# Kernel optimization log

Measured on AMD Instinct MI355X. Metric: run time of the kernel, lower is better.

Reference implementation:

```python
import jax, jax.numpy as jnp
import numpy as np

MAX_ITER = 10
EPSILON = 1e-4
B, N1, N2 = 64, 1024, 1024


def setup_inputs() -> dict:
    key = jax.random.key(0)
    k_s, k_r, k_c = jax.random.split(key, 3)
    s = jax.random.uniform(k_s, (B, N1, N2), dtype=jnp.float32)
    nrows = jax.random.randint(k_r, (B,), 512, N1 + 1, dtype=jnp.int32)
    ncols = jax.random.randint(k_c, (B,), 512, N2 + 1, dtype=jnp.int32)
    return {"s": s, "n1": N1, "n2": N2, "nrows": nrows, "ncols": ncols}


def reference(s, n1, n2, nrows, ncols):
    # s: [B, N1, N2] affinity; nrows/ncols: [B] valid sizes; n1/n2: static ints.
    b, r, c = s.shape
    row_mask = jnp.arange(r)[None, :] < nrows[:, None]          # [B, N1]
    col_mask = jnp.arange(c)[None, :] < ncols[:, None]          # [B, N2]
    valid = row_mask[:, :, None] & col_mask[:, None, :]         # [B, N1, N2]

    s = s + EPSILON
    # off-block zeroing (no-op when n1==N1, n2==N2, matching torch fill_(0))
    s = s.at[:, :n1, n2:].set(0.0)
    s = s.at[:, n1:, :n2].set(0.0)

    for i in range(MAX_ITER):
        if i % 2 == 1:
            # row sums over valid columns (s @ col_ones_block), broadcast over cols
            ssum = jnp.sum(jnp.where(col_mask[:, None, :], s, 0.0), axis=2, keepdims=True)
        else:
            # column sums over valid rows (row_ones_block @ s), broadcast over rows
            ssum = jnp.sum(jnp.where(row_mask[:, :, None], s, 0.0), axis=1, keepdims=True)
        denom = jnp.where(valid, jnp.broadcast_to(ssum, s.shape), 1.0)
        s = jnp.where(valid, s / denom, 0.0)  # tmp = 1/sum inside block, 0 outside
    return s
```

## Files before the change

### kernel.cpp

```cpp
#include <hip/hip_runtime.h>

#define EPS 1e-4f
#define BB 64
#define NN 1024

typedef _Float16 f16x8 __attribute__((ext_vector_type(8)));
typedef _Float16 f16x4 __attribute__((ext_vector_type(4)));

__global__ __launch_bounds__(256) void compress_colsum_k(
    const float* __restrict__ s, _Float16* __restrict__ A,
    const int* __restrict__ nrows, const int* __restrict__ ncols,
    float* __restrict__ partial)
{
    int chunk = blockIdx.x;
    int b = blockIdx.y;
    int nr = nrows[b], nc = ncols[b];
    int t = threadIdx.x;
    int j = t << 2;
    int i0 = chunk << 6;
    int i1 = min(i0 + 64, nr);
    const float* sb = s + ((size_t)b << 20) + j;
    _Float16* Ab = A + ((size_t)b << 20) + j;
    float a0 = 0.f, a1 = 0.f, a2 = 0.f, a3 = 0.f;
    if (j < nc) {
        for (int i = i0; i < i1; ++i) {
            float4 v = *(const float4*)(sb + ((size_t)i << 10));
            float m0 = (j + 0 < nc) ? v.x + EPS : 0.f;
            float m1 = (j + 1 < nc) ? v.y + EPS : 0.f;
            float m2 = (j + 2 < nc) ? v.z + EPS : 0.f;
            float m3 = (j + 3 < nc) ? v.w + EPS : 0.f;
            f16x4 h;
            h[0] = (_Float16)m0; h[1] = (_Float16)m1;
            h[2] = (_Float16)m2; h[3] = (_Float16)m3;
            a0 += (float)h[0]; a1 += (float)h[1];
            a2 += (float)h[2]; a3 += (float)h[3];
            *(f16x4*)(Ab + ((size_t)i << 10)) = h;
        }
    } else {
        f16x4 z = {};
        for (int i = i0; i < i1; ++i)
            *(f16x4*)(Ab + ((size_t)i << 10)) = z;
    }
    *(float4*)(partial + (((size_t)((chunk << 6) + b)) << 10) + j) =
        make_float4(a0, a1, a2, a3);
}

__global__ __launch_bounds__(256) void pair_k(
    const _Float16* __restrict__ A, const float* __restrict__ pin,
    const int* __restrict__ nrows, const int* __restrict__ ncols,
    float* __restrict__ pout)
{
    __shared__ float cs[NN];
    __shared__ float mg[4][NN];
    int chunk = blockIdx.x, b = blockIdx.y;
    int nr = nrows[b], nc = ncols[b];
    int t = threadIdx.x;
    {
        int j = t << 2;
        const float* pb = pin + ((size_t)b << 10) + j;
        float4 u = make_float4(0.f, 0.f, 0.f, 0.f);
#pragma unroll
        for (int k = 0; k < 16; ++k) {
            float4 p = *(const float4*)(pb + ((size_t)k << 16));
            u.x += p.x; u.y += p.y; u.z += p.z; u.w += p.w;
        }
        cs[j + 0] = (j + 0 < nc) ? 1.0f / u.x : 0.f;
        cs[j + 1] = (j + 1 < nc) ? 1.0f / u.y : 0.f;
        cs[j + 2] = (j + 2 < nc) ? 1.0f / u.z : 0.f;
        cs[j + 3] = (j + 3 < nc) ? 1.0f / u.w : 0.f;
    }
    __syncthreads();

    int w = t >> 6, lane = t & 63;
    int col0 = lane << 3;
    float4 c0a = *(const float4*)&cs[col0];
    float4 c0b = *(const float4*)&cs[col0 + 4];
    float4 c1a = *(const float4*)&cs[512 + col0];
    float4 c1b = *(const float4*)&cs[512 + col0 + 4];
    bool do1 = (512 + col0) < nc;

    float acc0[8] = {0.f, 0.f, 0.f, 0.f, 0.f, 0.f, 0.f, 0.f};
    float acc1[8] = {0.f, 0.f, 0.f, 0.f, 0.f, 0.f, 0.f, 0.f};
    const _Float16* Ab = A + ((size_t)b << 20);
    int i0 = chunk << 6;
    int iend = min(i0 + 64, nr);
    for (int i = i0 + w; i < iend; i += 4) {
        const _Float16* row = Ab + ((size_t)i << 10);
        f16x8 q0 = *(const f16x8*)(row + col0);
        f16x8 q1 = {};
        if (do1) q1 = *(const f16x8*)(row + 512 + col0);
        float f0[8], f1[8];
#pragma unroll
        for (int k = 0; k < 8; ++k) { f0[k] = (float)q0[k]; f1[k] = (float)q1[k]; }
        float sum = f0[0]*c0a.x + f0[1]*c0a.y + f0[2]*c0a.z + f0[3]*c0a.w
                  + f0[4]*c0b.x + f0[5]*c0b.y + f0[6]*c0b.z + f0[7]*c0b.w
                  + f1[0]*c1a.x + f1[1]*c1a.y + f1[2]*c1a.z + f1[3]*c1a.w
                  + f1[4]*c1b.x + f1[5]*c1b.y + f1[6]*c1b.z + f1[7]*c1b.w;
#pragma unroll
        for (int o = 32; o > 0; o >>= 1) sum += __shfl_xor(sum, o, 64);
        float ri = 1.0f / sum;
#pragma unroll
        for (int k = 0; k < 8; ++k) { acc0[k] += f0[k] * ri; acc1[k] += f1[k] * ri; }
    }
    *(float4*)&mg[w][col0]       = make_float4(acc0[0], acc0[1], acc0[2], acc0[3]);
    *(float4*)&mg[w][col0 + 4]   = make_float4(acc0[4], acc0[5], acc0[6], acc0[7]);
    *(float4*)&mg[w][512 + col0]     = make_float4(acc1[0], acc1[1], acc1[2], acc1[3]);
    *(float4*)&mg[w][512 + col0 + 4] = make_float4(acc1[4], acc1[5], acc1[6], acc1[7]);
    __syncthreads();
    int j = t << 2;
    float4 m = make_float4(0.f, 0.f, 0.f, 0.f);
#pragma unroll
    for (int ww = 0; ww < 4; ++ww) {
        float4 v = *(const float4*)&mg[ww][j];
        m.x += v.x; m.y += v.y; m.z += v.z; m.w += v.w;
    }
    *(float4*)(pout + (((size_t)((chunk << 6) + b)) << 10) + j) = m;
}

__global__ __launch_bounds__(256) void reduce_c_k(
    const float* __restrict__ partial, const int* __restrict__ ncols,
    float* __restrict__ c)
{
    int b = blockIdx.y;
    int j = (blockIdx.x << 8) + threadIdx.x;
    int nc = ncols[b];
    const float* pb = partial + ((size_t)b << 10) + j;
    float u = 0.f;
#pragma unroll
    for (int k = 0; k < 16; ++k) u += pb[(size_t)k << 16];
    c[(b << 10) + j] = (j < nc) ? 1.0f / u : 0.f;
}

__global__ __launch_bounds__(256) void finalize_k(
    const _Float16* __restrict__ A, const float* __restrict__ c,
    const int* __restrict__ nrows, float* __restrict__ out)
{
    __shared__ float red[4];
    int b = blockIdx.y, i = blockIdx.x;
    int nr = nrows[b];
    int t = threadIdx.x;
    int j = t << 2;
    size_t off = ((size_t)b << 20) + ((size_t)i << 10) + j;
    if (i >= nr) {
        *(float4*)(out + off) = make_float4(0.f, 0.f, 0.f, 0.f);
        return;
    }
    f16x4 h = *(const f16x4*)(A + off);
    float4 cv = *(const float4*)(c + (b << 10) + j);
    float4 p;
    p.x = (float)h[0] * cv.x;
    p.y = (float)h[1] * cv.y;
    p.z = (float)h[2] * cv.z;
    p.w = (float)h[3] * cv.w;
    float sum = (p.x + p.y) + (p.z + p.w);
#pragma unroll
    for (int o = 32; o > 0; o >>= 1) sum += __shfl_xor(sum, o, 64);
    int w = t >> 6, lane = t & 63;
    if (lane == 0) red[w] = sum;
    __syncthreads();
    float total = (red[0] + red[1]) + (red[2] + red[3]);
    float ri = 1.0f / total;
    *(float4*)(out + off) = make_float4(p.x * ri, p.y * ri, p.z * ri, p.w * ri);
}

extern "C" void kernel_launch(void* const* d_in, const int* in_sizes, int n_in,
                              void* d_out, int out_size, void* d_ws, size_t ws_size,
                              hipStream_t stream) {
    const float* s     = (const float*)d_in[0];
    const int*   nrows = (const int*)d_in[3];
    const int*   ncols = (const int*)d_in[4];
    float* out = (float*)d_out;

    _Float16* A  = (_Float16*)d_ws;
    float* pA    = (float*)((char*)d_ws + ((size_t)BB << 20) * sizeof(_Float16));
    float* pB    = pA + ((size_t)16 * BB * NN);
    float* c5    = pB + ((size_t)16 * BB * NN);

    compress_colsum_k<<<dim3(16, BB), 256, 0, stream>>>(s, A, nrows, ncols, pA);
    pair_k<<<dim3(16, BB), 256, 0, stream>>>(A, pA, nrows, ncols, pB);
    pair_k<<<dim3(16, BB), 256, 0, stream>>>(A, pB, nrows, ncols, pA);
    pair_k<<<dim3(16, BB), 256, 0, stream>>>(A, pA, nrows, ncols, pB);
    pair_k<<<dim3(16, BB), 256, 0, stream>>>(A, pB, nrows, ncols, pA);
    reduce_c_k<<<dim3(4, BB), 256, 0, stream>>>(pA, ncols, c5);
    finalize_k<<<dim3(NN, BB), 256, 0, stream>>>(A, c5, nrows, out);
}
```

Before: 565.3 us.

## Fuse final column reduction into finalize and process two rows per wave

Removes the separate reduce_c kernel by folding the partial column-sum reduction into a new finalize kernel that works on 64-row chunks per block, as pair_k does. The final pass now uses a 16x64 grid instead of 1024x64 blocks of one row each. Both pair_k and finalize process two rows per wave per iteration, interleaving the two shuffle reductions to expose more ILP and memory parallelism. The cost is more registers per thread, and each finalize block redundantly re-reduces the 16 partials.

```diff
diff --git a/kernel.cpp b/kernel.cpp
--- a/kernel.cpp
+++ b/kernel.cpp
@@ -84,26 +84,55 @@
     const _Float16* Ab = A + ((size_t)b << 20);
     int i0 = chunk << 6;
     int iend = min(i0 + 64, nr);
-    for (int i = i0 + w; i < iend; i += 4) {
-        const _Float16* row = Ab + ((size_t)i << 10);
-        f16x8 q0 = *(const f16x8*)(row + col0);
-        f16x8 q1 = {};
-        if (do1) q1 = *(const f16x8*)(row + 512 + col0);
-        float f0[8], f1[8];
-#pragma unroll
-        for (int k = 0; k < 8; ++k) { f0[k] = (float)q0[k]; f1[k] = (float)q1[k]; }
-        float sum = f0[0]*c0a.x + f0[1]*c0a.y + f0[2]*c0a.z + f0[3]*c0a.w
-                  + f0[4]*c0b.x + f0[5]*c0b.y + f0[6]*c0b.z + f0[7]*c0b.w
-                  + f1[0]*c1a.x + f1[1]*c1a.y + f1[2]*c1a.z + f1[3]*c1a.w
-                  + f1[4]*c1b.x + f1[5]*c1b.y + f1[6]*c1b.z + f1[7]*c1b.w;
-#pragma unroll
-        for (int o = 32; o > 0; o >>= 1) sum += __shfl_xor(sum, o, 64);
-        float ri = 1.0f / sum;
-#pragma unroll
-        for (int k = 0; k < 8; ++k) { acc0[k] += f0[k] * ri; acc1[k] += f1[k] * ri; }
-    }
-    *(float4*)&mg[w][col0]       = make_float4(acc0[0], acc0[1], acc0[2], acc0[3]);
-    *(float4*)&mg[w][col0 + 4]   = make_float4(acc0[4], acc0[5], acc0[6], acc0[7]);
+    for (int i = i0 + w; i < iend; i += 8) {
+        int ib = i + 4;
+        bool hasB = ib < iend;
+        const _Float16* rA = Ab + ((size_t)i << 10);
+        const _Float16* rB = Ab + ((size_t)(hasB ? ib : i) << 10);
+        f16x8 qa0 = *(const f16x8*)(rA + col0);
+        f16x8 qb0 = *(const f16x8*)(rB + col0);
+        f16x8 qa1 = {}; f16x8 qb1 = {};
+        if (do1) {
+            qa1 = *(const f16x8*)(rA + 512 + col0);
+            qb1 = *(const f16x8*)(rB + 512 + col0);
+        }
+        float fa0[8], fa1[8], fb0[8], fb1[8];
+#pragma unroll
+        for (int k = 0; k < 8; ++k) {
+            fa0[k] = (float)qa0[k]; fa1[k] = (float)qa1[k];
+            fb0[k] = (float)qb0[k]; fb1[k] = (float)qb1[k];
+        }
+        float sa, sb_;
+        {
+            float p0 = fa0[0]*c0a.x + fa0[1]*c0a.y + fa0[2]*c0a.z + fa0[3]*c0a.w;
+            float p1 = fa0[4]*c0b.x + fa0[5]*c0b.y + fa0[6]*c0b.z + fa0[7]*c0b.w;
+            float p2 = fa1[0]*c1a.x + fa1[1]*c1a.y + fa1[2]*c1a.z + fa1[3]*c1a.w;
+            float p3 = fa1[4]*c1b.x + fa1[5]*c1b.y + fa1[6]*c1b.z + fa1[7]*c1b.w;
+            sa = (p0 + p1) + (p2 + p3);
+        }
+        {
+            float p0 = fb0[0]*c0a.x + fb0[1]*c0a.y + fb0[2]*c0a.z + fb0[3]*c0a.w;
+            float p1 = fb0[4]*c0b.x + fb0[5]*c0b.y + fb0[6]*c0b.z + fb0[7]*c0b.w;
+            float p2 = fb1[0]*c1a.x + fb1[1]*c1a.y + fb1[2]*c1a.z + fb1[3]*c1a.w;
+            float p3 = fb1[4]*c1b.x + fb1[5]*c1b.y + fb1[6]*c1b.z + fb1[7]*c1b.w;
+            sb_ = (p0 + p1) + (p2 + p3);
+        }
+#pragma unroll
+        for (int o = 32; o > 0; o >>= 1) {
+            float ta = __shfl_xor(sa, o, 64);
+            float tb = __shfl_xor(sb_, o, 64);
+            sa += ta; sb_ += tb;
+        }
+        float ra = 1.0f / sa;
+        float rb = hasB ? (1.0f / sb_) : 0.f;
+#pragma unroll
+        for (int k = 0; k < 8; ++k) {
+            acc0[k] += fa0[k] * ra + fb0[k] * rb;
+            acc1[k] += fa1[k] * ra + fb1[k] * rb;
+        }
+    }
+    *(float4*)&mg[w][col0]           = make_float4(acc0[0], acc0[1], acc0[2], acc0[3]);
+    *(float4*)&mg[w][col0 + 4]       = make_float4(acc0[4], acc0[5], acc0[6], acc0[7]);
     *(float4*)&mg[w][512 + col0]     = make_float4(acc1[0], acc1[1], acc1[2], acc1[3]);
     *(float4*)&mg[w][512 + col0 + 4] = make_float4(acc1[4], acc1[5], acc1[6], acc1[7]);
     __syncthreads();
@@ -117,50 +146,116 @@
     *(float4*)(pout + (((size_t)((chunk << 6) + b)) << 10) + j) = m;
 }
 
-__global__ __launch_bounds__(256) void reduce_c_k(
-    const float* __restrict__ partial, const int* __restrict__ ncols,
-    float* __restrict__ c)
+__global__ __launch_bounds__(256) void finalize2_k(
+    const _Float16* __restrict__ A, const float* __restrict__ pin,
+    const int* __restrict__ nrows, const int* __restrict__ ncols,
+    float* __restrict__ out)
 {
-    int b = blockIdx.y;
-    int j = (blockIdx.x << 8) + threadIdx.x;
-    int nc = ncols[b];
-    const float* pb = partial + ((size_t)b << 10) + j;
-    float u = 0.f;
-#pragma unroll
-    for (int k = 0; k < 16; ++k) u += pb[(size_t)k << 16];
-    c[(b << 10) + j] = (j < nc) ? 1.0f / u : 0.f;
-}
-
-__global__ __launch_bounds__(256) void finalize_k(
-    const _Float16* __restrict__ A, const float* __restrict__ c,
-    const int* __restrict__ nrows, float* __restrict__ out)
-{
-    __shared__ float red[4];
-    int b = blockIdx.y, i = blockIdx.x;
-    int nr = nrows[b];
+    __shared__ float cs[NN];
+    int chunk = blockIdx.x, b = blockIdx.y;
+    int nr = nrows[b], nc = ncols[b];
     int t = threadIdx.x;
-    int j = t << 2;
-    size_t off = ((size_t)b << 20) + ((size_t)i << 10) + j;
-    if (i >= nr) {
-        *(float4*)(out + off) = make_float4(0.f, 0.f, 0.f, 0.f);
-        return;
-    }
-    f16x4 h = *(const f16x4*)(A + off);
-    float4 cv = *(const float4*)(c + (b << 10) + j);
-    float4 p;
-    p.x = (float)h[0] * cv.x;
-    p.y = (float)h[1] * cv.y;
-    p.z = (float)h[2] * cv.z;
-    p.w = (float)h[3] * cv.w;
-    float sum = (p.x + p.y) + (p.z + p.w);
-#pragma unroll
-    for (int o = 32; o > 0; o >>= 1) sum += __shfl_xor(sum, o, 64);
+    {
+        int j = t << 2;
+        const float* pb = pin + ((size_t)b << 10) + j;
+        float4 u = make_float4(0.f, 0.f, 0.f, 0.f);
+#pragma unroll
+        for (int k = 0; k < 16; ++k) {
+            float4 p = *(const float4*)(pb + ((size_t)k << 16));
+            u.x += p.x; u.y += p.y; u.z += p.z; u.w += p.w;
+        }
+        cs[j + 0] = (j + 0 < nc) ? 1.0f / u.x : 0.f;
+        cs[j + 1] = (j + 1 < nc) ? 1.0f / u.y : 0.f;
+        cs[j + 2] = (j + 2 < nc) ? 1.0f / u.z : 0.f;
+        cs[j + 3] = (j + 3 < nc) ? 1.0f / u.w : 0.f;
+    }
+    __syncthreads();
+
     int w = t >> 6, lane = t & 63;
-    if (lane == 0) red[w] = sum;
-    __syncthreads();
-    float total = (red[0] + red[1]) + (red[2] + red[3]);
-    float ri = 1.0f / total;
-    *(float4*)(out + off) = make_float4(p.x * ri, p.y * ri, p.z * ri, p.w * ri);
+    int col0 = lane << 3;
+    float4 c0a = *(const float4*)&cs[col0];
+    float4 c0b = *(const float4*)&cs[col0 + 4];
+    float4 c1a = *(const float4*)&cs[512 + col0];
+    float4 c1b = *(const float4*)&cs[512 + col0 + 4];
+    bool do1 = (512 + col0) < nc;
+
+    const _Float16* Ab = A + ((size_t)b << 20);
+    float* Ob = out + ((size_t)b << 20);
+    int i0 = chunk << 6;
+    int iend = min(i0 + 64, nr);
+    for (int i = i0 + w; i < iend; i += 8) {
+        int ib = i + 4;
+        bool hasB = ib < iend;
+        const _Float16* rA = Ab + ((size_t)i << 10);
+        const _Float16* rB = Ab + ((size_t)(hasB ? ib : i) << 10);
+        f16x8 qa0 = *(const f16x8*)(rA + col0);
+        f16x8 qb0 = *(const f16x8*)(rB + col0);
+        f16x8 qa1 = {}; f16x8 qb1 = {};
+        if (do1) {
+            qa1 = *(const f16x8*)(rA + 512 + col0);
+            qb1 = *(const f16x8*)(rB + 512 + col0);
+        }
+        float pa[16], pb2[16];
+        pa[0]  = (float)qa0[0]*c0a.x; pa[1]  = (float)qa0[1]*c0a.y;
+        pa[2]  = (float)qa0[2]*c0a.z; pa[3]  = (float)qa0[3]*c0a.w;
+        pa[4]  = (float)qa0[4]*c0b.x; pa[5]  = (float)qa0[5]*c0b.y;
+        pa[6]  = (float)qa0[6]*c0b.z; pa[7]  = (float)qa0[7]*c0b.w;
+        pa[8]  = (float)qa1[0]*c1a.x; pa[9]  = (float)qa1[1]*c1a.y;
+        pa[10] = (float)qa1[2]*c1a.z; pa[11] = (float)qa1[3]*c1a.w;
+        pa[12] = (float)qa1[4]*c1b.x; pa[13] = (float)qa1[5]*c1b.y;
+        pa[14] = (float)qa1[6]*c1b.z; pa[15] = (float)qa1[7]*c1b.w;
+        pb2[0]  = (float)qb0[0]*c0a.x; pb2[1]  = (float)qb0[1]*c0a.y;
+        pb2[2]  = (float)qb0[2]*c0a.z; pb2[3]  = (float)qb0[3]*c0a.w;
+        pb2[4]  = (float)qb0[4]*c0b.x; pb2[5]  = (float)qb0[5]*c0b.y;
+        pb2[6]  = (float)qb0[6]*c0b.z; pb2[7]  = (float)qb0[7]*c0b.w;
+        pb2[8]  = (float)qb1[0]*c1a.x; pb2[9]  = (float)qb1[1]*c1a.y;
+        pb2[10] = (float)qb1[2]*c1a.z; pb2[11] = (float)qb1[3]*c1a.w;
+        pb2[12] = (float)qb1[4]*c1b.x; pb2[13] = (float)qb1[5]*c1b.y;
+        pb2[14] = (float)qb1[6]*c1b.z; pb2[15] = (float)qb1[7]*c1b.w;
+        float sa, sb_;
+        {
+            float q0 = ((pa[0]+pa[1])+(pa[2]+pa[3])) + ((pa[4]+pa[5])+(pa[6]+pa[7]));
+            float q1 = ((pa[8]+pa[9])+(pa[10]+pa[11])) + ((pa[12]+pa[13])+(pa[14]+pa[15]));
+            sa = q0 + q1;
+        }
+        {
+            float q0 = ((pb2[0]+pb2[1])+(pb2[2]+pb2[3])) + ((pb2[4]+pb2[5])+(pb2[6]+pb2[7]));
+            float q1 = ((pb2[8]+pb2[9])+(pb2[10]+pb2[11])) + ((pb2[12]+pb2[13])+(pb2[14]+pb2[15]));
+            sb_ = q0 + q1;
+        }
+#pragma unroll
+        for (int o = 32; o > 0; o >>= 1) {
+            float ta = __shfl_xor(sa, o, 64);
+            float tb = __shfl_xor(sb_, o, 64);
+            sa += ta; sb_ += tb;
+        }
+        float ra = 1.0f / sa;
+        {
+            float* o = Ob + ((size_t)i << 10);
+            *(float4*)(o + col0)           = make_float4(pa[0]*ra,  pa[1]*ra,  pa[2]*ra,  pa[3]*ra);
+            *(float4*)(o + col0 + 4)       = make_float4(pa[4]*ra,  pa[5]*ra,  pa[6]*ra,  pa[7]*ra);
+            *(float4*)(o + 512 + col0)     = make_float4(pa[8]*ra,  pa[9]*ra,  pa[10]*ra, pa[11]*ra);
+            *(float4*)(o + 512 + col0 + 4) = make_float4(pa[12]*ra, pa[13]*ra, pa[14]*ra, pa[15]*ra);
+        }
+        if (hasB) {
+            float rb = 1.0f / sb_;
+            float* o = Ob + ((size_t)ib << 10);
+            *(float4*)(o + col0)           = make_float4(pb2[0]*rb,  pb2[1]*rb,  pb2[2]*rb,  pb2[3]*rb);
+            *(float4*)(o + col0 + 4)       = make_float4(pb2[4]*rb,  pb2[5]*rb,  pb2[6]*rb,  pb2[7]*rb);
+            *(float4*)(o + 512 + col0)     = make_float4(pb2[8]*rb,  pb2[9]*rb,  pb2[10]*rb, pb2[11]*rb);
+            *(float4*)(o + 512 + col0 + 4) = make_float4(pb2[12]*rb, pb2[13]*rb, pb2[14]*rb, pb2[15]*rb);
+        }
+    }
+    for (int i = i0 + w; i < i0 + 64; i += 4) {
+        if (i >= nr) {
+            float* o = Ob + ((size_t)i << 10);
+            float4 z = make_float4(0.f, 0.f, 0.f, 0.f);
+            *(float4*)(o + col0)           = z;
+            *(float4*)(o + col0 + 4)       = z;
+            *(float4*)(o + 512 + col0)     = z;
+            *(float4*)(o + 512 + col0 + 4) = z;
+        }
+    }
 }
 
 extern "C" void kernel_launch(void* const* d_in, const int* in_sizes, int n_in,
@@ -174,13 +269,11 @@
     _Float16* A  = (_Float16*)d_ws;
     float* pA    = (float*)((char*)d_ws + ((size_t)BB << 20) * sizeof(_Float16));
     float* pB    = pA + ((size_t)16 * BB * NN);
-    float* c5    = pB + ((size_t)16 * BB * NN);
 
     compress_colsum_k<<<dim3(16, BB), 256, 0, stream>>>(s, A, nrows, ncols, pA);
     pair_k<<<dim3(16, BB), 256, 0, stream>>>(A, pA, nrows, ncols, pB);
     pair_k<<<dim3(16, BB), 256, 0, stream>>>(A, pB, nrows, ncols, pA);
     pair_k<<<dim3(16, BB), 256, 0, stream>>>(A, pA, nrows, ncols, pB);
     pair_k<<<dim3(16, BB), 256, 0, stream>>>(A, pB, nrows, ncols, pA);
-    reduce_c_k<<<dim3(4, BB), 256, 0, stream>>>(pA, ncols, c5);
-    finalize_k<<<dim3(NN, BB), 256, 0, stream>>>(A, c5, nrows, out);
-}
+    finalize2_k<<<dim3(16, BB), 256, 0, stream>>>(A, pA, nrows, ncols, out);
+}
```

After: 567.9 us. No clear change (+0.4%).

## Fuse all Sinkhorn stages into one persistent kernel with grid barriers

Applied to the files above, without the earlier changes.

Replaces the seven separate kernel launches with a single persistent kernel of 256 blocks of 1024 threads (four blocks per batch). Stages are separated by atomic-counter grid barriers, and the final row normalisation is folded into the same kernel. The goal is to remove launch gaps and shrink the partial-sum buffers. In exchange it relies on all 256 blocks being co-resident, which risks deadlock otherwise, and it uses less parallelism per stage with spin-waits at each barrier.

```diff
diff --git a/kernel.cpp b/kernel.cpp
--- a/kernel.cpp
+++ b/kernel.cpp
@@ -7,160 +7,206 @@
 typedef _Float16 f16x8 __attribute__((ext_vector_type(8)));
 typedef _Float16 f16x4 __attribute__((ext_vector_type(4)));
 
-__global__ __launch_bounds__(256) void compress_colsum_k(
+__device__ __forceinline__ void grid_barrier(unsigned* bar, int slot,
+                                             unsigned nblk) {
+    __syncthreads();
+    if (threadIdx.x == 0) {
+        __threadfence();
+        __hip_atomic_fetch_add(&bar[slot], 1u, __ATOMIC_ACQ_REL,
+                               __HIP_MEMORY_SCOPE_AGENT);
+        while (__hip_atomic_load(&bar[slot], __ATOMIC_ACQUIRE,
+                                 __HIP_MEMORY_SCOPE_AGENT) < nblk) {
+            __builtin_amdgcn_s_sleep(8);
+        }
+        __threadfence();
+    }
+    __syncthreads();
+}
+
+__global__ __launch_bounds__(1024) void sinkhorn_fused(
     const float* __restrict__ s, _Float16* __restrict__ A,
     const int* __restrict__ nrows, const int* __restrict__ ncols,
-    float* __restrict__ partial)
+    float* __restrict__ p0, float* __restrict__ p1,
+    unsigned* __restrict__ bar, float* __restrict__ out)
 {
-    int chunk = blockIdx.x;
-    int b = blockIdx.y;
+    __shared__ float cs[NN];
+    __shared__ float mg[8][NN];
+
+    const unsigned NBLK = 256;
+    int g = blockIdx.x;
+    int q = g & 3, b = g >> 2;
     int nr = nrows[b], nc = ncols[b];
     int t = threadIdx.x;
-    int j = t << 2;
-    int i0 = chunk << 6;
-    int i1 = min(i0 + 64, nr);
-    const float* sb = s + ((size_t)b << 20) + j;
-    _Float16* Ab = A + ((size_t)b << 20) + j;
-    float a0 = 0.f, a1 = 0.f, a2 = 0.f, a3 = 0.f;
-    if (j < nc) {
-        for (int i = i0; i < i1; ++i) {
-            float4 v = *(const float4*)(sb + ((size_t)i << 10));
-            float m0 = (j + 0 < nc) ? v.x + EPS : 0.f;
-            float m1 = (j + 1 < nc) ? v.y + EPS : 0.f;
-            float m2 = (j + 2 < nc) ? v.z + EPS : 0.f;
-            float m3 = (j + 3 < nc) ? v.w + EPS : 0.f;
-            f16x4 h;
-            h[0] = (_Float16)m0; h[1] = (_Float16)m1;
-            h[2] = (_Float16)m2; h[3] = (_Float16)m3;
-            a0 += (float)h[0]; a1 += (float)h[1];
-            a2 += (float)h[2]; a3 += (float)h[3];
-            *(f16x4*)(Ab + ((size_t)i << 10)) = h;
-        }
-    } else {
-        f16x4 z = {};
-        for (int i = i0; i < i1; ++i)
-            *(f16x4*)(Ab + ((size_t)i << 10)) = z;
-    }
-    *(float4*)(partial + (((size_t)((chunk << 6) + b)) << 10) + j) =
-        make_float4(a0, a1, a2, a3);
-}
-
-__global__ __launch_bounds__(256) void pair_k(
-    const _Float16* __restrict__ A, const float* __restrict__ pin,
-    const int* __restrict__ nrows, const int* __restrict__ ncols,
-    float* __restrict__ pout)
-{
-    __shared__ float cs[NN];
-    __shared__ float mg[4][NN];
-    int chunk = blockIdx.x, b = blockIdx.y;
-    int nr = nrows[b], nc = ncols[b];
-    int t = threadIdx.x;
-    {
-        int j = t << 2;
-        const float* pb = pin + ((size_t)b << 10) + j;
-        float4 u = make_float4(0.f, 0.f, 0.f, 0.f);
-#pragma unroll
-        for (int k = 0; k < 16; ++k) {
-            float4 p = *(const float4*)(pb + ((size_t)k << 16));
-            u.x += p.x; u.y += p.y; u.z += p.z; u.w += p.w;
-        }
-        cs[j + 0] = (j + 0 < nc) ? 1.0f / u.x : 0.f;
-        cs[j + 1] = (j + 1 < nc) ? 1.0f / u.y : 0.f;
-        cs[j + 2] = (j + 2 < nc) ? 1.0f / u.z : 0.f;
-        cs[j + 3] = (j + 3 < nc) ? 1.0f / u.w : 0.f;
-    }
-    __syncthreads();
-
     int w = t >> 6, lane = t & 63;
     int col0 = lane << 3;
-    float4 c0a = *(const float4*)&cs[col0];
-    float4 c0b = *(const float4*)&cs[col0 + 4];
-    float4 c1a = *(const float4*)&cs[512 + col0];
-    float4 c1b = *(const float4*)&cs[512 + col0 + 4];
-    bool do1 = (512 + col0) < nc;
-
-    float acc0[8] = {0.f, 0.f, 0.f, 0.f, 0.f, 0.f, 0.f, 0.f};
-    float acc1[8] = {0.f, 0.f, 0.f, 0.f, 0.f, 0.f, 0.f, 0.f};
+    int tq = t >> 8, tj = t & 255;
+    int j4 = tj << 2;
     const _Float16* Ab = A + ((size_t)b << 20);
-    int i0 = chunk << 6;
-    int iend = min(i0 + 64, nr);
-    for (int i = i0 + w; i < iend; i += 4) {
-        const _Float16* row = Ab + ((size_t)i << 10);
-        f16x8 q0 = *(const f16x8*)(row + col0);
-        f16x8 q1 = {};
-        if (do1) q1 = *(const f16x8*)(row + 512 + col0);
-        float f0[8], f1[8];
-#pragma unroll
-        for (int k = 0; k < 8; ++k) { f0[k] = (float)q0[k]; f1[k] = (float)q1[k]; }
-        float sum = f0[0]*c0a.x + f0[1]*c0a.y + f0[2]*c0a.z + f0[3]*c0a.w
-                  + f0[4]*c0b.x + f0[5]*c0b.y + f0[6]*c0b.z + f0[7]*c0b.w
-                  + f1[0]*c1a.x + f1[1]*c1a.y + f1[2]*c1a.z + f1[3]*c1a.w
-                  + f1[4]*c1b.x + f1[5]*c1b.y + f1[6]*c1b.z + f1[7]*c1b.w;
-#pragma unroll
-        for (int o = 32; o > 0; o >>= 1) sum += __shfl_xor(sum, o, 64);
-        float ri = 1.0f / sum;
-#pragma unroll
-        for (int k = 0; k < 8; ++k) { acc0[k] += f0[k] * ri; acc1[k] += f1[k] * ri; }
-    }
-    *(float4*)&mg[w][col0]       = make_float4(acc0[0], acc0[1], acc0[2], acc0[3]);
-    *(float4*)&mg[w][col0 + 4]   = make_float4(acc0[4], acc0[5], acc0[6], acc0[7]);
-    *(float4*)&mg[w][512 + col0]     = make_float4(acc1[0], acc1[1], acc1[2], acc1[3]);
-    *(float4*)&mg[w][512 + col0 + 4] = make_float4(acc1[4], acc1[5], acc1[6], acc1[7]);
+    size_t poffQ = ((size_t)((q << 6) + b)) << 10;
+
+    {
+        int chunk = (q << 2) + tq;
+        int r0 = chunk << 6;
+        int r1 = min(r0 + 64, nr);
+        const float* sb = s + ((size_t)b << 20) + j4;
+        _Float16* Aw = A + ((size_t)b << 20) + j4;
+        float a0 = 0.f, a1 = 0.f, a2 = 0.f, a3 = 0.f;
+        if (j4 < nc) {
+            for (int i = r0; i < r1; ++i) {
+                float4 v = *(const float4*)(sb + ((size_t)i << 10));
+                float m0 = (j4 + 0 < nc) ? v.x + EPS : 0.f;
+                float m1 = (j4 + 1 < nc) ? v.y + EPS : 0.f;
+                float m2 = (j4 + 2 < nc) ? v.z + EPS : 0.f;
+                float m3 = (j4 + 3 < nc) ? v.w + EPS : 0.f;
+                f16x4 h;
+                h[0] = (_Float16)m0; h[1] = (_Float16)m1;
+                h[2] = (_Float16)m2; h[3] = (_Float16)m3;
+                a0 += (float)h[0]; a1 += (float)h[1];
+                a2 += (float)h[2]; a3 += (float)h[3];
+                *(f16x4*)(Aw + ((size_t)i << 10)) = h;
+            }
+        } else {
+            f16x4 z = {};
+            for (int i = r0; i < r1; ++i)
+                *(f16x4*)(Aw + ((size_t)i << 10)) = z;
+        }
+        *(float4*)&mg[tq][j4] = make_float4(a0, a1, a2, a3);
+        __syncthreads();
+        if (t < 256) {
+            int jj = t << 2;
+            float4 m = make_float4(0.f, 0.f, 0.f, 0.f);
+#pragma unroll
+            for (int k = 0; k < 4; ++k) {
+                float4 v = *(const float4*)&mg[k][jj];
+                m.x += v.x; m.y += v.y; m.z += v.z; m.w += v.w;
+            }
+            *(float4*)(p0 + poffQ + jj) = m;
+        }
+    }
+    grid_barrier(bar, 0, NBLK);
+
+    const float* pin = p0;
+    float* pout = p1;
+    for (int it = 0; it < 4; ++it) {
+        {
+            const float* pb = pin + ((size_t)b << 10) + t;
+            float u = 0.f;
+#pragma unroll
+            for (int k = 0; k < 4; ++k) u += pb[(size_t)k << 16];
+            cs[t] = (t < nc) ? 1.0f / u : 0.f;
+        }
+        __syncthreads();
+
+        float4 c0a = *(const float4*)&cs[col0];
+        float4 c0b = *(const float4*)&cs[col0 + 4];
+        float4 c1a = *(const float4*)&cs[512 + col0];
+        float4 c1b = *(const float4*)&cs[512 + col0 + 4];
+        bool do1 = (512 + col0) < nc;
+
+        float acc0[8] = {0.f, 0.f, 0.f, 0.f, 0.f, 0.f, 0.f, 0.f};
+        float acc1[8] = {0.f, 0.f, 0.f, 0.f, 0.f, 0.f, 0.f, 0.f};
+        int base = (q << 8) + (w << 4);
+        int iend = min(base + 16, nr);
+        for (int i = base; i < iend; ++i) {
+            const _Float16* row = Ab + ((size_t)i << 10);
+            f16x8 q0 = *(const f16x8*)(row + col0);
+            f16x8 q1 = {};
+            if (do1) q1 = *(const f16x8*)(row + 512 + col0);
+            float f0[8], f1[8];
+#pragma unroll
+            for (int k = 0; k < 8; ++k) { f0[k] = (float)q0[k]; f1[k] = (float)q1[k]; }
+            float p0s = f0[0]*c0a.x + f0[1]*c0a.y + f0[2]*c0a.z + f0[3]*c0a.w;
+            float p1s = f0[4]*c0b.x + f0[5]*c0b.y + f0[6]*c0b.z + f0[7]*c0b.w;
+            float p2s = f1[0]*c1a.x + f1[1]*c1a.y + f1[2]*c1a.z + f1[3]*c1a.w;
+            float p3s = f1[4]*c1b.x + f1[5]*c1b.y + f1[6]*c1b.z + f1[7]*c1b.w;
+            float sum = (p0s + p1s) + (p2s + p3s);
+#pragma unroll
+            for (int o = 32; o > 0; o >>= 1) sum += __shfl_xor(sum, o, 64);
+            float ri = 1.0f / sum;
+#pragma unroll
+            for (int k = 0; k < 8; ++k) { acc0[k] += f0[k] * ri; acc1[k] += f1[k] * ri; }
+        }
+        if (w >= 8) {
+            int ww = w - 8;
+            *(float4*)&mg[ww][col0]           = make_float4(acc0[0], acc0[1], acc0[2], acc0[3]);
+            *(float4*)&mg[ww][col0 + 4]       = make_float4(acc0[4], acc0[5], acc0[6], acc0[7]);
+            *(float4*)&mg[ww][512 + col0]     = make_float4(acc1[0], acc1[1], acc1[2], acc1[3]);
+            *(float4*)&mg[ww][512 + col0 + 4] = make_float4(acc1[4], acc1[5], acc1[6], acc1[7]);
+        }
+        __syncthreads();
+        if (w < 8) {
+            float4 v;
+            v = *(const float4*)&mg[w][col0];
+            *(float4*)&mg[w][col0]           = make_float4(v.x+acc0[0], v.y+acc0[1], v.z+acc0[2], v.w+acc0[3]);
+            v = *(const float4*)&mg[w][col0 + 4];
+            *(float4*)&mg[w][col0 + 4]       = make_float4(v.x+acc0[4], v.y+acc0[5], v.z+acc0[6], v.w+acc0[7]);
+            v = *(const float4*)&mg[w][512 + col0];
+            *(float4*)&mg[w][512 + col0]     = make_float4(v.x+acc1[0], v.y+acc1[1], v.z+acc1[2], v.w+acc1[3]);
+            v = *(const float4*)&mg[w][512 + col0 + 4];
+            *(float4*)&mg[w][512 + col0 + 4] = make_float4(v.x+acc1[4], v.y+acc1[5], v.z+acc1[6], v.w+acc1[7]);
+        }
+        __syncthreads();
+        {
+            float m = 0.f;
+#pragma unroll
+            for (int k = 0; k < 8; ++k) m += mg[k][t];
+            pout[poffQ + t] = m;
+        }
+        grid_barrier(bar, 1 + it, NBLK);
+        const float* tmp = pout; pout = (float*)pin; pin = tmp;
+    }
+
+    {
+        const float* pb = pin + ((size_t)b << 10) + t;
+        float u = 0.f;
+#pragma unroll
+        for (int k = 0; k < 4; ++k) u += pb[(size_t)k << 16];
+        cs[t] = (t < nc) ? 1.0f / u : 0.f;
+    }
     __syncthreads();
-    int j = t << 2;
-    float4 m = make_float4(0.f, 0.f, 0.f, 0.f);
-#pragma unroll
-    for (int ww = 0; ww < 4; ++ww) {
-        float4 v = *(const float4*)&mg[ww][j];
-        m.x += v.x; m.y += v.y; m.z += v.z; m.w += v.w;
-    }
-    *(float4*)(pout + (((size_t)((chunk << 6) + b)) << 10) + j) = m;
-}
-
-__global__ __launch_bounds__(256) void reduce_c_k(
-    const float* __restrict__ partial, const int* __restrict__ ncols,
-    float* __restrict__ c)
-{
-    int b = blockIdx.y;
-    int j = (blockIdx.x << 8) + threadIdx.x;
-    int nc = ncols[b];
-    const float* pb = partial + ((size_t)b << 10) + j;
-    float u = 0.f;
-#pragma unroll
-    for (int k = 0; k < 16; ++k) u += pb[(size_t)k << 16];
-    c[(b << 10) + j] = (j < nc) ? 1.0f / u : 0.f;
-}
-
-__global__ __launch_bounds__(256) void finalize_k(
-    const _Float16* __restrict__ A, const float* __restrict__ c,
-    const int* __restrict__ nrows, float* __restrict__ out)
-{
-    __shared__ float red[4];
-    int b = blockIdx.y, i = blockIdx.x;
-    int nr = nrows[b];
-    int t = threadIdx.x;
-    int j = t << 2;
-    size_t off = ((size_t)b << 20) + ((size_t)i << 10) + j;
-    if (i >= nr) {
-        *(float4*)(out + off) = make_float4(0.f, 0.f, 0.f, 0.f);
-        return;
-    }
-    f16x4 h = *(const f16x4*)(A + off);
-    float4 cv = *(const float4*)(c + (b << 10) + j);
-    float4 p;
-    p.x = (float)h[0] * cv.x;
-    p.y = (float)h[1] * cv.y;
-    p.z = (float)h[2] * cv.z;
-    p.w = (float)h[3] * cv.w;
-    float sum = (p.x + p.y) + (p.z + p.w);
-#pragma unroll
-    for (int o = 32; o > 0; o >>= 1) sum += __shfl_xor(sum, o, 64);
-    int w = t >> 6, lane = t & 63;
-    if (lane == 0) red[w] = sum;
-    __syncthreads();
-    float total = (red[0] + red[1]) + (red[2] + red[3]);
-    float ri = 1.0f / total;
-    *(float4*)(out + off) = make_float4(p.x * ri, p.y * ri, p.z * ri, p.w * ri);
+    {
+        float4 c0a = *(const float4*)&cs[col0];
+        float4 c0b = *(const float4*)&cs[col0 + 4];
+        float4 c1a = *(const float4*)&cs[512 + col0];
+        float4 c1b = *(const float4*)&cs[512 + col0 + 4];
+        bool do1 = (512 + col0) < nc;
+        float* Ob = out + ((size_t)b << 20);
+        int base = (q << 8) + (w << 4);
+        for (int i = base; i < base + 16; ++i) {
+            float* o = Ob + ((size_t)i << 10);
+            if (i < nr) {
+                const _Float16* row = Ab + ((size_t)i << 10);
+                f16x8 q0 = *(const f16x8*)(row + col0);
+                f16x8 q1 = {};
+                if (do1) q1 = *(const f16x8*)(row + 512 + col0);
+                float p[16];
+                p[0]  = (float)q0[0]*c0a.x; p[1]  = (float)q0[1]*c0a.y;
+                p[2]  = (float)q0[2]*c0a.z; p[3]  = (float)q0[3]*c0a.w;
+                p[4]  = (float)q0[4]*c0b.x; p[5]  = (float)q0[5]*c0b.y;
+                p[6]  = (float)q0[6]*c0b.z; p[7]  = (float)q0[7]*c0b.w;
+                p[8]  = (float)q1[0]*c1a.x; p[9]  = (float)q1[1]*c1a.y;
+                p[10] = (float)q1[2]*c1a.z; p[11] = (float)q1[3]*c1a.w;
+                p[12] = (float)q1[4]*c1b.x; p[13] = (float)q1[5]*c1b.y;
+                p[14] = (float)q1[6]*c1b.z; p[15] = (float)q1[7]*c1b.w;
+                float s0 = ((p[0]+p[1])+(p[2]+p[3])) + ((p[4]+p[5])+(p[6]+p[7]));
+                float s1 = ((p[8]+p[9])+(p[10]+p[11])) + ((p[12]+p[13])+(p[14]+p[15]));
+                float sum = s0 + s1;
+#pragma unroll
+                for (int o2 = 32; o2 > 0; o2 >>= 1) sum += __shfl_xor(sum, o2, 64);
+                float ri = 1.0f / sum;
+                *(float4*)(o + col0)           = make_float4(p[0]*ri,  p[1]*ri,  p[2]*ri,  p[3]*ri);
+                *(float4*)(o + col0 + 4)       = make_float4(p[4]*ri,  p[5]*ri,  p[6]*ri,  p[7]*ri);
+                *(float4*)(o + 512 + col0)     = make_float4(p[8]*ri,  p[9]*ri,  p[10]*ri, p[11]*ri);
+                *(float4*)(o + 512 + col0 + 4) = make_float4(p[12]*ri, p[13]*ri, p[14]*ri, p[15]*ri);
+            } else {
+                float4 z = make_float4(0.f, 0.f, 0.f, 0.f);
+                *(float4*)(o + col0)           = z;
+                *(float4*)(o + col0 + 4)       = z;
+                *(float4*)(o + 512 + col0)     = z;
+                *(float4*)(o + 512 + col0 + 4) = z;
+            }
+        }
+    }
 }
 
 extern "C" void kernel_launch(void* const* d_in, const int* in_sizes, int n_in,
@@ -173,14 +219,11 @@
 
     _Float16* A  = (_Float16*)d_ws;
     float* pA    = (float*)((char*)d_ws + ((size_t)BB << 20) * sizeof(_Float16));
-    float* pB    = pA + ((size_t)16 * BB * NN);
-    float* c5    = pB + ((size_t)16 * BB * NN);
-
-    compress_colsum_k<<<dim3(16, BB), 256, 0, stream>>>(s, A, nrows, ncols, pA);
-    pair_k<<<dim3(16, BB), 256, 0, stream>>>(A, pA, nrows, ncols, pB);
-    pair_k<<<dim3(16, BB), 256, 0, stream>>>(A, pB, nrows, ncols, pA);
-    pair_k<<<dim3(16, BB), 256, 0, stream>>>(A, pA, nrows, ncols, pB);
-    pair_k<<<dim3(16, BB), 256, 0, stream>>>(A, pB, nrows, ncols, pA);
-    reduce_c_k<<<dim3(4, BB), 256, 0, stream>>>(pA, ncols, c5);
-    finalize_k<<<dim3(NN, BB), 256, 0, stream>>>(A, c5, nrows, out);
+    float* pB    = pA + ((size_t)4 * BB * NN);
+    unsigned* bar = (unsigned*)(pB + ((size_t)4 * BB * NN));
+
+    hipMemsetAsync(bar, 0, 8 * sizeof(unsigned), stream);
+
+    sinkhorn_fused<<<dim3(256), dim3(1024), 0, stream>>>(
+        s, A, nrows, ncols, pA, pB, bar, out);
 }
```

Result: slower. 782.5 us (+38.4%).
